# Performance work log

Hardware: AMD Instinct MI355X
Metric: run time of the kernel (lower is better)

## Reference

```python
import jax, jax.numpy as jnp
import numpy as np

M, N, D = 4096, 50000, 64
BANDWIDTH_INIT = 1.0  # coeff is frozen at init-time bandwidth in the torch module


def setup_inputs() -> dict:
    key = jax.random.key(0)
    k1, k2 = jax.random.split(key)
    x = jax.random.normal(k1, (M, D), dtype=jnp.float32)
    X = jax.random.normal(k2, (N, D), dtype=jnp.float32)
    bandwidth = jnp.ones((1,), dtype=jnp.float32)
    return {"x": x, "X": X, "bandwidth": bandwidth}


def reference(x, X, bandwidth):
    n, d = X.shape
    # coeff computed from *initial* bandwidth (Python float in torch __init__) -> constant
    coeff = np.float32(-np.log(n) - np.log(2.0 * np.pi) * d / 2.0
                       - np.log(BANDWIDTH_INIT) * d)
    b = bandwidth[0]
    # squared euclidean distances via norms + matmul (avoids explicit diff tensor)
    x2 = jnp.sum(x * x, axis=-1, keepdims=True)            # [M, 1]
    X2 = jnp.sum(X * X, axis=-1)                           # [N]
    cross = x @ X.T                                        # [M, N]
    d2 = jnp.maximum(x2 + X2[None, :] - 2.0 * cross, 0.0)  # [M, N]
    logits = d2 / (-2.0 * b * b)
    return jax.nn.logsumexp(logits, axis=1) + coeff        # [M]
```

## Files before the change

### kernel.cpp

```cpp
#include <hip/hip_runtime.h>
#include <hip/hip_bf16.h>
#include <math.h>

#define NSPLIT 24
#define MROWS  128

typedef __attribute__((ext_vector_type(8))) short short8;
typedef __attribute__((ext_vector_type(4))) float f32x4;

__device__ __forceinline__ short f2bf(float f) {
    __hip_bfloat16 h = __float2bfloat16(f);
    return __builtin_bit_cast(short, h);
}

__global__ __launch_bounds__(256) void kde_prep(
    const float* __restrict__ x, const float* __restrict__ Xg,
    const float* __restrict__ bw,
    short* __restrict__ Xb, float* __restrict__ Eq,
    short* __restrict__ xb, float* __restrict__ x2q, int M, int N)
{
    const int gid = blockIdx.x * 256 + threadIdx.x;
    const int row = gid >> 3;
    const int sub = gid & 7;
    if (row >= M + N) return;

    const float b = bw[0];
    const float q = -1.4426950408889634f / (2.f * b * b);
    const float s2q = -2.f * q;

    const float* src;
    short* dst;
    float sc;
    if (row < N) { src = Xg + (size_t)row * 64;     dst = Xb + (size_t)row * 64;     sc = 1.f; }
    else         { src = x  + (size_t)(row-N) * 64; dst = xb + (size_t)(row-N) * 64; sc = s2q; }

    float4 v0 = ((const float4*)(src + sub * 8))[0];
    float4 v1 = ((const float4*)(src + sub * 8))[1];

    float ss = v0.x*v0.x + v0.y*v0.y + v0.z*v0.z + v0.w*v0.w
             + v1.x*v1.x + v1.y*v1.y + v1.z*v1.z + v1.w*v1.w;
    ss += __shfl_xor(ss, 1);
    ss += __shfl_xor(ss, 2);
    ss += __shfl_xor(ss, 4);

    short8 o;
    o[0]=f2bf(v0.x*sc); o[1]=f2bf(v0.y*sc); o[2]=f2bf(v0.z*sc); o[3]=f2bf(v0.w*sc);
    o[4]=f2bf(v1.x*sc); o[5]=f2bf(v1.y*sc); o[6]=f2bf(v1.z*sc); o[7]=f2bf(v1.w*sc);
    *(short8*)(dst + sub * 8) = o;

    if (sub == 0) {
        if (row < N) Eq[row] = exp2f(ss * q);
        else         x2q[row - N] = ss * q;
    }
}

__global__ __launch_bounds__(256, 2) void kde_main6(
    const short* __restrict__ Xb, const float* __restrict__ Eq,
    const short* __restrict__ xb,
    float* __restrict__ partial, int M, int N, int NB)
{
    const int tid  = threadIdx.x;
    const int lane = tid & 63;
    const int wave = tid >> 6;
    const int l15  = lane & 15;
    const int kq   = lane >> 4;

    const int L      = blockIdx.x;
    const int split  = (L & 7) + 8 * (L / (8 * NB));
    const int mblock = (L >> 3) % NB;
    const int rowbase = mblock * MROWS;

    const int T    = (N + 63) >> 6;
    const int base = T / NSPLIT;
    const int remu = T % NSPLIT;
    const int it0  = split * base + min(split, remu);
    const int cnt  = base + (split < remu ? 1 : 0);
    const bool maskedLast = (it0 + cnt == T) && ((N & 63) != 0);
    const int nfull = cnt - (maskedLast ? 1 : 0);

    short8 afrag[8][2];
    #pragma unroll
    for (int rf = 0; rf < 8; ++rf) {
        const short* p = xb + (size_t)(rowbase + rf*16 + l15) * 64 + kq * 8;
        afrag[rf][0] = *(const short8*)(p);
        afrag[rf][1] = *(const short8*)(p + 32);
    }

    const f32x4 zero4 = {0.f, 0.f, 0.f, 0.f};

    float s[8][4];
    #pragma unroll
    for (int rf = 0; rf < 8; ++rf)
        #pragma unroll
        for (int r = 0; r < 4; ++r) s[rf][r] = 0.f;

    const short* pB = Xb + (size_t)(it0*64 + wave*16 + l15) * 64 + kq * 8;
    const float* pE = Eq + it0*64 + wave*16 + l15;
    const size_t strideB = (size_t)64 * 64;

    f32x4 acc[8];
    short8 Ba0, Ba1, Bb0, Bb1;
    float  Ea, Eb;

    auto LOADA = [&]() {
        Ba0 = *(const short8*)(pB);
        Ba1 = *(const short8*)(pB + 32);
        Ea  = *pE;
        pB += strideB; pE += 64;
    };
    auto LOADB = [&]() {
        Bb0 = *(const short8*)(pB);
        Bb1 = *(const short8*)(pB + 32);
        Eb  = *pE;
        pB += strideB; pE += 64;
    };

    auto MFMAPH = [&](short8 B0, short8 B1) {
        #pragma unroll
        for (int rf = 0; rf < 8; ++rf) {
            f32x4 a = __builtin_amdgcn_mfma_f32_16x16x32_bf16(afrag[rf][0], B0, zero4, 0, 0, 0);
            acc[rf] = __builtin_amdgcn_mfma_f32_16x16x32_bf16(afrag[rf][1], B1, a, 0, 0, 0);
        }
    };
    auto EXPPH = [&](float E) {
        #pragma unroll
        for (int rf = 0; rf < 8; ++rf)
            #pragma unroll
            for (int r = 0; r < 4; ++r)
                s[rf][r] = fmaf(E, __builtin_amdgcn_exp2f(acc[rf][r]), s[rf][r]);
    };

    if (nfull > 0) LOADA();
    for (int it = 0; it < nfull; it += 2) {
        if (it + 1 < nfull) LOADB();
        __builtin_amdgcn_sched_barrier(0);
        MFMAPH(Ba0, Ba1);
        EXPPH(Ea);
        if (it + 1 < nfull) {
            if (it + 2 < nfull) LOADA();
            __builtin_amdgcn_sched_barrier(0);
            MFMAPH(Bb0, Bb1);
            EXPPH(Eb);
        }
    }

    if (maskedLast) {
        const int col = (it0 + cnt - 1)*64 + wave*16 + l15;
        const int c   = min(col, N - 1);
        const short* p = Xb + (size_t)c * 64 + kq * 8;
        Ba0 = *(const short8*)(p);
        Ba1 = *(const short8*)(p + 32);
        Ea  = (col < N) ? Eq[c] : 0.f;
        MFMAPH(Ba0, Ba1);
        EXPPH(Ea);
    }

    float t[8][4];
    #pragma unroll
    for (int rf = 0; rf < 8; ++rf)
        #pragma unroll
        for (int r = 0; r < 4; ++r) {
            float v = s[rf][r];
            v += __shfl_xor(v, 1);
            v += __shfl_xor(v, 2);
            v += __shfl_xor(v, 4);
            v += __shfl_xor(v, 8);
            t[rf][r] = v;
        }

    __shared__ float red[4][MROWS];
    if (l15 == 0) {
        #pragma unroll
        for (int rf = 0; rf < 8; ++rf)
            #pragma unroll
            for (int r = 0; r < 4; ++r)
                red[wave][rf*16 + kq*4 + r] = t[rf][r];
    }
    __syncthreads();
    if (tid < MROWS) {
        partial[(size_t)split * M + rowbase + tid] =
            red[0][tid] + red[1][tid] + red[2][tid] + red[3][tid];
    }
}

__global__ __launch_bounds__(256) void kde_combine2(
    const float* __restrict__ ws, const float* __restrict__ x2q,
    float* __restrict__ out, int M, int nsplit, float coeff)
{
    int i = blockIdx.x * 256 + threadIdx.x;
    if (i < M) {
        float t = 0.f;
        for (int s = 0; s < nsplit; ++s) t += ws[(size_t)s * M + i];
        out[i] = fmaf(0.6931471805599453f, x2q[i], logf(t) + coeff);
    }
}

__global__ __launch_bounds__(256) void kde_main_fb(
    const float* __restrict__ x, const float* __restrict__ Xg,
    const float* __restrict__ bw, float* __restrict__ ws,
    float* __restrict__ out, int M, int N, int nsplit, float coeff)
{
    const int tid  = threadIdx.x;
    const int lane = tid & 63;
    const int wave = tid >> 6;
    const int l15  = lane & 15;
    const int kq   = lane >> 4;
    const int rowbase = blockIdx.x * 64;
    const int split   = blockIdx.y;
    const int chunk   = (N + nsplit - 1) / nsplit;
    const int colstart = split * chunk;
    const int colend   = min(colstart + chunk, N);

    __shared__ float lds_x2[64];
    __shared__ float red[4][64];

    if (tid < 64) {
        const float* xp = x + (size_t)(rowbase + tid) * 64;
        float ssum = 0.f;
        #pragma unroll
        for (int k = 0; k < 16; ++k) {
            float4 v = ((const float4*)xp)[k];
            ssum += v.x*v.x + v.y*v.y + v.z*v.z + v.w*v.w;
        }
        lds_x2[tid] = ssum;
    }

    short8 afrag[4][2];
    #pragma unroll
    for (int rf = 0; rf < 4; ++rf) {
        const float* xp = x + (size_t)(rowbase + rf*16 + l15) * 64;
        #pragma unroll
        for (int kf = 0; kf < 2; ++kf) {
            const float* p = xp + kf*32 + kq*8;
            float4 v0 = ((const float4*)p)[0];
            float4 v1 = ((const float4*)p)[1];
            short8 a;
            a[0]=f2bf(v0.x); a[1]=f2bf(v0.y); a[2]=f2bf(v0.z); a[3]=f2bf(v0.w);
            a[4]=f2bf(v1.x); a[5]=f2bf(v1.y); a[6]=f2bf(v1.z); a[7]=f2bf(v1.w);
            afrag[rf][kf] = a;
        }
    }
    __syncthreads();

    float xa[4][4];
    #pragma unroll
    for (int rf = 0; rf < 4; ++rf)
        #pragma unroll
        for (int r = 0; r < 4; ++r)
            xa[rf][r] = lds_x2[rf*16 + kq*4 + r];

    const float b = bw[0];
    const float q = -1.4426950408889634f / (2.f * b * b);

    float s[4][4];
    #pragma unroll
    for (int rf = 0; rf < 4; ++rf)
        #pragma unroll
        for (int r = 0; r < 4; ++r) s[rf][r] = 0.f;

    const int span  = colend - colstart;
    const int niter = (span + 63) / 64;

    for (int it = 0; it < niter; ++it) {
        const int col  = colstart + it*64 + wave*16 + l15;
        const int colc = min(col, N - 1);
        const bool valid = (col < colend);

        const float* Xp = Xg + (size_t)colc * 64;
        float4 v0 = ((const float4*)(Xp + kq*8))[0];
        float4 v1 = ((const float4*)(Xp + kq*8))[1];
        float4 v2 = ((const float4*)(Xp + 32 + kq*8))[0];
        float4 v3 = ((const float4*)(Xp + 32 + kq*8))[1];

        float pa = v0.x*v0.x + v0.y*v0.y + v0.z*v0.z + v0.w*v0.w
                 + v1.x*v1.x + v1.y*v1.y + v1.z*v1.z + v1.w*v1.w
                 + v2.x*v2.x + v2.y*v2.y + v2.z*v2.z + v2.w*v2.w
                 + v3.x*v3.x + v3.y*v3.y + v3.z*v3.z + v3.w*v3.w;
        pa += __shfl_xor(pa, 16);
        pa += __shfl_xor(pa, 32);

        short8 bb0, bb1;
        bb0[0]=f2bf(v0.x); bb0[1]=f2bf(v0.y); bb0[2]=f2bf(v0.z); bb0[3]=f2bf(v0.w);
        bb0[4]=f2bf(v1.x); bb0[5]=f2bf(v1.y); bb0[6]=f2bf(v1.z); bb0[7]=f2bf(v1.w);
        bb1[0]=f2bf(v2.x); bb1[1]=f2bf(v2.y); bb1[2]=f2bf(v2.z); bb1[3]=f2bf(v2.w);
        bb1[4]=f2bf(v3.x); bb1[5]=f2bf(v3.y); bb1[6]=f2bf(v3.z); bb1[7]=f2bf(v3.w);

        #pragma unroll
        for (int rf = 0; rf < 4; ++rf) {
            f32x4 acc = {0.f, 0.f, 0.f, 0.f};
            acc = __builtin_amdgcn_mfma_f32_16x16x32_bf16(afrag[rf][0], bb0, acc, 0, 0, 0);
            acc = __builtin_amdgcn_mfma_f32_16x16x32_bf16(afrag[rf][1], bb1, acc, 0, 0, 0);
            #pragma unroll
            for (int r = 0; r < 4; ++r) {
                float d2 = fmaxf(xa[rf][r] + pa - 2.f*acc[r], 0.f);
                float e = valid ? __builtin_amdgcn_exp2f(d2 * q) : 0.f;
                s[rf][r] += e;
            }
        }
    }

    #pragma unroll
    for (int rf = 0; rf < 4; ++rf)
        #pragma unroll
        for (int r = 0; r < 4; ++r) {
            float v = s[rf][r];
            v += __shfl_xor(v, 1);
            v += __shfl_xor(v, 2);
            v += __shfl_xor(v, 4);
            v += __shfl_xor(v, 8);
            s[rf][r] = v;
        }

    __syncthreads();
    if (l15 == 0) {
        #pragma unroll
        for (int rf = 0; rf < 4; ++rf)
            #pragma unroll
            for (int r = 0; r < 4; ++r)
                red[wave][rf*16 + kq*4 + r] = s[rf][r];
    }
    __syncthreads();

    if (tid < 64) {
        float tot = red[0][tid] + red[1][tid] + red[2][tid] + red[3][tid];
        if (nsplit == 1) out[rowbase + tid] = logf(tot) + coeff;
        else             ws[(size_t)split * M + rowbase + tid] = tot;
    }
}

__global__ __launch_bounds__(256) void kde_combine_fb(
    const float* __restrict__ ws, float* __restrict__ out,
    int M, int nsplit, float coeff)
{
    int i = blockIdx.x * 256 + threadIdx.x;
    if (i < M) {
        float t = 0.f;
        for (int s = 0; s < nsplit; ++s) t += ws[(size_t)s * M + i];
        out[i] = logf(t) + coeff;
    }
}

extern "C" void kernel_launch(void* const* d_in, const int* in_sizes, int n_in,
                              void* d_out, int out_size, void* d_ws, size_t ws_size,
                              hipStream_t stream) {
    const float* x  = (const float*)d_in[0];
    const float* Xg = (const float*)d_in[1];
    const float* bw = (const float*)d_in[2];
    float* out = (float*)d_out;

    const int M = in_sizes[0] / 64;
    const int N = in_sizes[1] / 64;
    const float coeff = -logf((float)N) - logf(2.f * (float)M_PI) * 32.f;

    auto align256 = [](size_t v) { return (v + 255) & ~(size_t)255; };
    const size_t szXb   = align256((size_t)N * 64 * sizeof(short));
    const size_t szxb   = align256((size_t)M * 64 * sizeof(short));
    const size_t szEq   = align256((size_t)N * sizeof(float));
    const size_t szx2q  = align256((size_t)M * sizeof(float));
    const size_t szPart = align256((size_t)NSPLIT * M * sizeof(float));
    const size_t need   = szXb + szxb + szEq + szx2q + szPart;

    if (ws_size >= need && (M % MROWS) == 0) {
        char* w = (char*)d_ws;
        short* Xb   = (short*)(w);
        short* xb   = (short*)(w + szXb);
        float* Eq   = (float*)(w + szXb + szxb);
        float* x2q  = (float*)(w + szXb + szxb + szEq);
        float* part = (float*)(w + szXb + szxb + szEq + szx2q);

        const int totalRows = M + N;
        kde_prep<<<(totalRows * 8 + 255) / 256, 256, 0, stream>>>(
            x, Xg, bw, Xb, Eq, xb, x2q, M, N);

        const int NB = M / MROWS;
        kde_main6<<<NB * NSPLIT, 256, 0, stream>>>(Xb, Eq, xb, part, M, N, NB);

        kde_combine2<<<(M + 255) / 256, 256, 0, stream>>>(part, x2q, out, M, NSPLIT, coeff);
    } else {
        int nsplit = 8;
        if (ws_size < (size_t)nsplit * M * sizeof(float)) nsplit = 1;
        dim3 grid(M / 64, nsplit);
        kde_main_fb<<<grid, 256, 0, stream>>>(x, Xg, bw, (float*)d_ws, out, M, N, nsplit, coeff);
        if (nsplit > 1)
            kde_combine_fb<<<(M + 255) / 256, 256, 0, stream>>>((const float*)d_ws, out, M, nsplit, coeff);
    }
}
```

Baseline: 56.50 us.

## Software-pipeline MFMA and exp across tiles with double accumulators; reduce split count

Restructures the main loop so the MFMA for the next column tile is issued alongside the exp2/accumulate of the previous tile's results, using two accumulator sets (accA/accB) with prologue and epilogue handling. This aims to overlap matrix-core work with transcendental VALU work instead of running them serially. NSPLIT also drops from 24 to 16, which changes grid size and per-block work and gives fewer partials to combine. The extra accumulator registers raise register pressure and may hurt occupancy or cause spills.

```diff
diff --git a/kernel.cpp b/kernel.cpp
--- a/kernel.cpp
+++ b/kernel.cpp
@@ -2,7 +2,7 @@
 #include <hip/hip_bf16.h>
 #include <math.h>
 
-#define NSPLIT 24
+#define NSPLIT 16
 #define MROWS  128
 
 typedef __attribute__((ext_vector_type(8))) short short8;
@@ -54,7 +54,7 @@
     }
 }
 
-__global__ __launch_bounds__(256, 2) void kde_main6(
+__global__ __launch_bounds__(256, 2) void kde_main7(
     const short* __restrict__ Xb, const float* __restrict__ Eq,
     const short* __restrict__ xb,
     float* __restrict__ partial, int M, int N, int NB)
@@ -98,7 +98,7 @@
     const float* pE = Eq + it0*64 + wave*16 + l15;
     const size_t strideB = (size_t)64 * 64;
 
-    f32x4 acc[8];
+    f32x4 accA[8], accB[8];
     short8 Ba0, Ba1, Bb0, Bb1;
     float  Ea, Eb;
 
@@ -115,32 +115,52 @@
         pB += strideB; pE += 64;
     };
 
-    auto MFMAPH = [&](short8 B0, short8 B1) {
+    auto MFMA_EXP = [&](short8 B0, short8 B1, f32x4 (&dst)[8],
+                        const f32x4 (&src)[8], float E) {
         #pragma unroll
         for (int rf = 0; rf < 8; ++rf) {
             f32x4 a = __builtin_amdgcn_mfma_f32_16x16x32_bf16(afrag[rf][0], B0, zero4, 0, 0, 0);
-            acc[rf] = __builtin_amdgcn_mfma_f32_16x16x32_bf16(afrag[rf][1], B1, a, 0, 0, 0);
+            dst[rf]  = __builtin_amdgcn_mfma_f32_16x16x32_bf16(afrag[rf][1], B1, a, 0, 0, 0);
+            #pragma unroll
+            for (int r = 0; r < 4; ++r)
+                s[rf][r] = fmaf(E, __builtin_amdgcn_exp2f(src[rf][r]), s[rf][r]);
         }
     };
-    auto EXPPH = [&](float E) {
+    auto MFMA_ONLY = [&](short8 B0, short8 B1, f32x4 (&dst)[8]) {
+        #pragma unroll
+        for (int rf = 0; rf < 8; ++rf) {
+            f32x4 a = __builtin_amdgcn_mfma_f32_16x16x32_bf16(afrag[rf][0], B0, zero4, 0, 0, 0);
+            dst[rf]  = __builtin_amdgcn_mfma_f32_16x16x32_bf16(afrag[rf][1], B1, a, 0, 0, 0);
+        }
+    };
+    auto EXP_ONLY = [&](const f32x4 (&src)[8], float E) {
         #pragma unroll
         for (int rf = 0; rf < 8; ++rf)
             #pragma unroll
             for (int r = 0; r < 4; ++r)
-                s[rf][r] = fmaf(E, __builtin_amdgcn_exp2f(acc[rf][r]), s[rf][r]);
+                s[rf][r] = fmaf(E, __builtin_amdgcn_exp2f(src[rf][r]), s[rf][r]);
     };
 
-    if (nfull > 0) LOADA();
-    for (int it = 0; it < nfull; it += 2) {
-        if (it + 1 < nfull) LOADB();
-        __builtin_amdgcn_sched_barrier(0);
-        MFMAPH(Ba0, Ba1);
-        EXPPH(Ea);
-        if (it + 1 < nfull) {
-            if (it + 2 < nfull) LOADA();
-            __builtin_amdgcn_sched_barrier(0);
-            MFMAPH(Bb0, Bb1);
-            EXPPH(Eb);
+    if (nfull > 0) {
+        LOADA();
+        if (nfull > 1) LOADB();
+        MFMA_ONLY(Ba0, Ba1, accA);
+        float EAc = Ea;
+
+        int it = 1;
+        for (; it + 1 < nfull; it += 2) {
+            LOADA();
+            MFMA_EXP(Bb0, Bb1, accB, accA, EAc);
+            float EBc = Eb;
+            if (it + 2 < nfull) LOADB();
+            MFMA_EXP(Ba0, Ba1, accA, accB, EBc);
+            EAc = Ea;
+        }
+        if (it < nfull) {
+            MFMA_EXP(Bb0, Bb1, accB, accA, EAc);
+            EXP_ONLY(accB, Eb);
+        } else {
+            EXP_ONLY(accA, EAc);
         }
     }
 
@@ -151,8 +171,8 @@
         Ba0 = *(const short8*)(p);
         Ba1 = *(const short8*)(p + 32);
         Ea  = (col < N) ? Eq[c] : 0.f;
-        MFMAPH(Ba0, Ba1);
-        EXPPH(Ea);
+        MFMA_ONLY(Ba0, Ba1, accA);
+        EXP_ONLY(accA, Ea);
     }
 
     float t[8][4];
@@ -373,7 +393,7 @@
             x, Xg, bw, Xb, Eq, xb, x2q, M, N);
 
         const int NB = M / MROWS;
-        kde_main6<<<NB * NSPLIT, 256, 0, stream>>>(Xb, Eq, xb, part, M, N, NB);
+        kde_main7<<<NB * NSPLIT, 256, 0, stream>>>(Xb, Eq, xb, part, M, N, NB);
 
         kde_combine2<<<(M + 255) / 256, 256, 0, stream>>>(part, x2q, out, M, NSPLIT, coeff);
     } else {
```

Result: faster. 52.24 us (-7.5%).

## Stream B tiles into LDS via async global_load_lds double buffering

Applied to the files above, without the earlier changes.

Replaces direct register loads of the X tiles and exp weights with asynchronous global-to-LDS loads into a per-wave double buffer, using an XOR swizzle to avoid bank conflicts and explicit vmcnt/lgkmcnt waits. Launch bounds are raised to three blocks per SIMD so fewer registers are held for prefetched B fragments and more waves fit. The aim is to hide global load latency behind the MFMA and exp work. It adds LDS traffic and hand-placed wait counts, which are fragile if the compiler emits other memory ops in between.

```diff
diff --git a/kernel.cpp b/kernel.cpp
--- a/kernel.cpp
+++ b/kernel.cpp
@@ -7,6 +7,9 @@
 
 typedef __attribute__((ext_vector_type(8))) short short8;
 typedef __attribute__((ext_vector_type(4))) float f32x4;
+
+#define AS1 __attribute__((address_space(1)))
+#define AS3 __attribute__((address_space(3)))
 
 __device__ __forceinline__ short f2bf(float f) {
     __hip_bfloat16 h = __float2bfloat16(f);
@@ -54,7 +57,7 @@
     }
 }
 
-__global__ __launch_bounds__(256, 2) void kde_main6(
+__global__ __launch_bounds__(256, 3) void kde_main10(
     const short* __restrict__ Xb, const float* __restrict__ Eq,
     const short* __restrict__ xb,
     float* __restrict__ partial, int M, int N, int NB)
@@ -78,6 +81,10 @@
     const bool maskedLast = (it0 + cnt == T) && ((N & 63) != 0);
     const int nfull = cnt - (maskedLast ? 1 : 0);
 
+    __shared__ short ldsB[4][2][1024];
+    __shared__ float ldsE[4][2][16];
+    __shared__ float red[4][MROWS];
+
     short8 afrag[8][2];
     #pragma unroll
     for (int rf = 0; rf < 8; ++rf) {
@@ -94,32 +101,35 @@
         #pragma unroll
         for (int r = 0; r < 4; ++r) s[rf][r] = 0.f;
 
-    const short* pB = Xb + (size_t)(it0*64 + wave*16 + l15) * 64 + kq * 8;
-    const float* pE = Eq + it0*64 + wave*16 + l15;
-    const size_t strideB = (size_t)64 * 64;
-
     f32x4 acc[8];
-    short8 Ba0, Ba1, Bb0, Bb1;
-    float  Ea, Eb;
-
-    auto LOADA = [&]() {
-        Ba0 = *(const short8*)(pB);
-        Ba1 = *(const short8*)(pB + 32);
-        Ea  = *pE;
-        pB += strideB; pE += 64;
-    };
-    auto LOADB = [&]() {
-        Bb0 = *(const short8*)(pB);
-        Bb1 = *(const short8*)(pB + 32);
-        Eb  = *pE;
-        pB += strideB; pE += 64;
+
+    auto STAGE = [&](int kabs, int c) {
+        const int colb = (it0 + kabs) * 64 + wave * 16;
+        #pragma unroll
+        for (int i = 0; i < 2; ++i) {
+            const int colr = i*8 + (lane >> 3);
+            const int seg  = lane & 7;
+            const char* src = (const char*)Xb
+                + (((size_t)(colb + colr)) << 7)
+                + (((seg ^ (colr & 7))) << 4);
+            __builtin_amdgcn_global_load_lds(
+                (const AS1 char*)src,
+                (AS3 char*)((char*)&ldsB[wave][c][0] + i * 1024),
+                16, 0, 0);
+        }
+        if (lane < 16) {
+            __builtin_amdgcn_global_load_lds(
+                (const AS1 char*)(const char*)(Eq + colb + lane),
+                (AS3 char*)(char*)&ldsE[wave][c][0],
+                4, 0, 0);
+        }
     };
 
     auto MFMAPH = [&](short8 B0, short8 B1) {
         #pragma unroll
         for (int rf = 0; rf < 8; ++rf) {
             f32x4 a = __builtin_amdgcn_mfma_f32_16x16x32_bf16(afrag[rf][0], B0, zero4, 0, 0, 0);
-            acc[rf] = __builtin_amdgcn_mfma_f32_16x16x32_bf16(afrag[rf][1], B1, a, 0, 0, 0);
+            acc[rf]  = __builtin_amdgcn_mfma_f32_16x16x32_bf16(afrag[rf][1], B1, a, 0, 0, 0);
         }
     };
     auto EXPPH = [&](float E) {
@@ -130,29 +140,44 @@
                 s[rf][r] = fmaf(E, __builtin_amdgcn_exp2f(acc[rf][r]), s[rf][r]);
     };
 
-    if (nfull > 0) LOADA();
-    for (int it = 0; it < nfull; it += 2) {
-        if (it + 1 < nfull) LOADB();
+    auto ITER = [&](int kabs, int c) {
+        if (kabs + 1 < nfull) asm volatile("s_waitcnt vmcnt(3)" ::: "memory");
+        else                  asm volatile("s_waitcnt vmcnt(0)" ::: "memory");
         __builtin_amdgcn_sched_barrier(0);
-        MFMAPH(Ba0, Ba1);
-        EXPPH(Ea);
-        if (it + 1 < nfull) {
-            if (it + 2 < nfull) LOADA();
-            __builtin_amdgcn_sched_barrier(0);
-            MFMAPH(Bb0, Bb1);
-            EXPPH(Eb);
-        }
-    }
+
+        const char* bb = (const char*)&ldsB[wave][c][0];
+        short8 B0 = *(const short8*)(bb + l15*128 + ((kq       ^ (l15 & 7)) << 4));
+        short8 B1 = *(const short8*)(bb + l15*128 + (((kq + 4) ^ (l15 & 7)) << 4));
+        float  E  = ldsE[wave][c][l15];
+
+        MFMAPH(B0, B1);
+
+        asm volatile("s_waitcnt lgkmcnt(0)" ::: "memory");
+        __builtin_amdgcn_sched_barrier(0);
+        if (kabs + 2 < nfull) STAGE(kabs + 2, c);
+
+        EXPPH(E);
+    };
+
+    if (nfull >= 1) STAGE(0, 0);
+    if (nfull >= 2) STAGE(1, 1);
+    int k = 0;
+    for (; k + 1 < nfull; k += 2) {
+        ITER(k, 0);
+        ITER(k + 1, 1);
+    }
+    if (k < nfull) ITER(k, 0);
 
     if (maskedLast) {
+        asm volatile("s_waitcnt vmcnt(0)" ::: "memory");
         const int col = (it0 + cnt - 1)*64 + wave*16 + l15;
         const int c   = min(col, N - 1);
         const short* p = Xb + (size_t)c * 64 + kq * 8;
-        Ba0 = *(const short8*)(p);
-        Ba1 = *(const short8*)(p + 32);
-        Ea  = (col < N) ? Eq[c] : 0.f;
-        MFMAPH(Ba0, Ba1);
-        EXPPH(Ea);
+        short8 B0 = *(const short8*)(p);
+        short8 B1 = *(const short8*)(p + 32);
+        float  E  = (col < N) ? Eq[c] : 0.f;
+        MFMAPH(B0, B1);
+        EXPPH(E);
     }
 
     float t[8][4];
@@ -168,7 +193,6 @@
             t[rf][r] = v;
         }
 
-    __shared__ float red[4][MROWS];
     if (l15 == 0) {
         #pragma unroll
         for (int rf = 0; rf < 8; ++rf)
@@ -373,7 +397,7 @@
             x, Xg, bw, Xb, Eq, xb, x2q, M, N);
 
         const int NB = M / MROWS;
-        kde_main6<<<NB * NSPLIT, 256, 0, stream>>>(Xb, Eq, xb, part, M, N, NB);
+        kde_main10<<<NB * NSPLIT, 256, 0, stream>>>(Xb, Eq, xb, part, M, N, NB);
 
         kde_combine2<<<(M + 255) / 256, 256, 0, stream>>>(part, x2q, out, M, NSPLIT, coeff);
     } else {
```

After: 88.51 us. 56.7% more time.
